# Kernel tuning notes

Measured on AMD Instinct MI355X. Metric: run time of the kernel, lower is better.

## Reference

```python
import jax, jax.numpy as jnp
import numpy as np

INPUT_SIZE = 64
HIDDEN_SIZE = 128
OUTPUT_SIZE = 64


def setup_inputs() -> dict:
    key = jax.random.key(0)
    ks = jax.random.split(key, 7)
    B, T = 256, 2048
    x = jax.random.normal(ks[0], (B, T, INPUT_SIZE), dtype=jnp.float32)
    s_in = 1.0 / np.sqrt(INPUT_SIZE)
    s_h = 1.0 / np.sqrt(HIDDEN_SIZE)
    Wx_w = jax.random.uniform(ks[1], (HIDDEN_SIZE, INPUT_SIZE), minval=-s_in, maxval=s_in, dtype=jnp.float32)
    Wx_b = jax.random.uniform(ks[2], (HIDDEN_SIZE,), minval=-s_in, maxval=s_in, dtype=jnp.float32)
    Wh_w = jax.random.uniform(ks[3], (HIDDEN_SIZE, HIDDEN_SIZE), minval=-s_h, maxval=s_h, dtype=jnp.float32)
    Wh_b = jax.random.uniform(ks[4], (HIDDEN_SIZE,), minval=-s_h, maxval=s_h, dtype=jnp.float32)
    fc_w = jax.random.uniform(ks[5], (OUTPUT_SIZE, HIDDEN_SIZE), minval=-s_h, maxval=s_h, dtype=jnp.float32)
    fc_b = jax.random.uniform(ks[6], (OUTPUT_SIZE,), minval=-s_h, maxval=s_h, dtype=jnp.float32)
    return {"x": x, "Wx_w": Wx_w, "Wx_b": Wx_b, "Wh_w": Wh_w, "Wh_b": Wh_b, "fc_w": fc_w, "fc_b": fc_b}


def reference(x, Wx_w, Wx_b, Wh_w, Wh_b, fc_w, fc_b):
    B = x.shape[0]
    # Precompute the input projection for all timesteps in one big GEMM;
    # the recurrence itself is a scan over time (sequential dependency).
    xt_proj = jnp.einsum('bti,hi->bth', x, Wx_w) + Wx_b  # [B, T, H]

    def step(h, xp):
        h = jnp.tanh(xp + h @ Wh_w.T + Wh_b)
        return h, None

    h0 = jnp.zeros((B, HIDDEN_SIZE), dtype=x.dtype)
    h_final, _ = jax.lax.scan(step, h0, jnp.swapaxes(xt_proj, 0, 1))  # scan over T
    out = h_final @ fc_w.T + fc_b  # [B, O]
    return jax.nn.softmax(out, axis=1)
```

## Files before the change

### kernel.cpp

```cpp
#include <hip/hip_runtime.h>

#define BATCH 256
#define TSTEPS 2048
#define INSZ 64
#define HID 128
#define OUTSZ 64
#define NTHR 512
#define CHUNK 32
#define NCHUNK (TSTEPS / CHUNK)

typedef float v2f __attribute__((ext_vector_type(2)));
typedef float v4f __attribute__((ext_vector_type(4)));

#define AS1 __attribute__((address_space(1)))
#define AS3 __attribute__((address_space(3)))

template <int CTRL>
__device__ __forceinline__ float dppf(float v) {
  return __int_as_float(__builtin_amdgcn_update_dpp(
      0, __float_as_int(v), CTRL, 0xF, 0xF, true));
}
#define DPP_XOR1 0xB1
#define DPP_XOR2 0x4E
#define DPP_XOR15 0x140
#define DPP_XOR8 0x128

__device__ __forceinline__ v2f pk_mul(v2f a, v2f b) {
  v2f d; asm("v_pk_mul_f32 %0, %1, %2" : "=v"(d) : "v"(a), "v"(b)); return d;
}
__device__ __forceinline__ v2f pk_fma(v2f a, v2f b, v2f c) {
  v2f d; asm("v_pk_fma_f32 %0, %1, %2, %3" : "=v"(d) : "v"(a), "v"(b), "v"(c)); return d;
}

__launch_bounds__(NTHR, 1)
__global__ void rnn_dpp512_kernel(const float* __restrict__ x,
                                  const float* __restrict__ Wx_w,
                                  const float* __restrict__ Wx_b,
                                  const float* __restrict__ Wh_w,
                                  const float* __restrict__ Wh_b,
                                  const float* __restrict__ fc_w,
                                  const float* __restrict__ fc_b,
                                  float* __restrict__ out) {
  const int b = blockIdx.x;
  const int tid = threadIdx.x;
  const int s = tid & 15;
  const int g = tid >> 4;
  const int s0 = s & 1, s1 = (s >> 1) & 1, s2 = (s >> 2) & 1;
  const int c = (s0 ^ s2) | ((s1 ^ s2) << 1);
  const int jf = 4 * g + c;
  const int jp = jf + ((jf >> 3) << 2);

  __shared__ __align__(16) float hA[192], hB[192];
  __shared__ __align__(16) float xsm[2][CHUNK * INSZ];

  v2f wh2[4][4], wx2[4][2];
#pragma unroll
  for (int m = 0; m < 4; ++m) {
    const int row = 4 * g + (m ^ c);
    const float* p = Wh_w + row * HID + 8 * s;
    v4f t0 = *(const v4f*)p;
    v4f t1 = *(const v4f*)(p + 4);
    wh2[m][0] = (v2f){t0.x, t0.y};
    wh2[m][1] = (v2f){t0.z, t0.w};
    wh2[m][2] = (v2f){t1.x, t1.y};
    wh2[m][3] = (v2f){t1.z, t1.w};
    const float* q = Wx_w + row * INSZ + 4 * s;
    v4f t2 = *(const v4f*)q;
    wx2[m][0] = (v2f){t2.x, t2.y};
    wx2[m][1] = (v2f){t2.z, t2.w};
  }
  const float bc = Wx_b[jf] + Wh_b[jf];

  const float* xg = x + (size_t)b * TSTEPS * INSZ;

  if (tid < 192) hA[tid] = 0.f;

  {
    const AS1 float* gp = (const AS1 float*)(xg + tid * 4);
    AS3 float* d = (AS3 float*)(&xsm[0][(tid >> 6) * 256]);
    __builtin_amdgcn_global_load_lds(gp, d, 16, 0, 0);
  }
  asm volatile("s_waitcnt vmcnt(0) lgkmcnt(0)\ns_barrier" ::: "memory");

  for (int tc = 0; tc < NCHUNK; ++tc) {
#pragma unroll
    for (int m = 0; m < 4; ++m) {
#pragma unroll
      for (int kk = 0; kk < 4; ++kk) asm("" : "+v"(wh2[m][kk]));
#pragma unroll
      for (int kk = 0; kk < 2; ++kk) asm("" : "+v"(wx2[m][kk]));
    }
    if (tc + 1 < NCHUNK) {
      const AS1 float* gp =
          (const AS1 float*)(xg + (size_t)(tc + 1) * CHUNK * INSZ + tid * 4);
      AS3 float* d = (AS3 float*)(&xsm[(tc + 1) & 1][(tid >> 6) * 256]);
      __builtin_amdgcn_global_load_lds(gp, d, 16, 0, 0);
    }
    const float* xc = xsm[tc & 1];
    v4f xcur = *(const v4f*)&xc[4 * s];

#pragma unroll
    for (int ts = 0; ts < CHUNK; ++ts) {
      const float* hin = (ts & 1) ? hB : hA;
      float* hout = (ts & 1) ? hA : hB;

      const float* hp = hin + 12 * s;
      v4f h0 = *(const v4f*)hp;
      v4f h1 = *(const v4f*)(hp + 4);

      v4f xnext;
      if (ts + 1 < CHUNK) xnext = *(const v4f*)&xc[(ts + 1) * INSZ + 4 * s];

      v2f xx0 = (v2f){xcur.x, xcur.y}, xx1 = (v2f){xcur.z, xcur.w};
      v2f hx0 = (v2f){h0.x, h0.y}, hx1 = (v2f){h0.z, h0.w};
      v2f hx2 = (v2f){h1.x, h1.y}, hx3 = (v2f){h1.z, h1.w};

      float a0, a1, a2, a3;
      float* aptr[4] = {&a0, &a1, &a2, &a3};
#pragma unroll
      for (int m = 0; m < 4; ++m) {
        v2f acc = pk_mul(wx2[m][0], xx0);
        acc = pk_fma(wx2[m][1], xx1, acc);
        acc = pk_fma(wh2[m][0], hx0, acc);
        acc = pk_fma(wh2[m][1], hx1, acc);
        acc = pk_fma(wh2[m][2], hx2, acc);
        acc = pk_fma(wh2[m][3], hx3, acc);
        *aptr[m] = acc.x + acc.y;
      }

      float b0 = a0 + dppf<DPP_XOR1>(a1);
      float b1 = a2 + dppf<DPP_XOR1>(a3);
      float w  = b0 + dppf<DPP_XOR2>(b1);
      float u  = w + dppf<DPP_XOR15>(w);
      float z  = u + dppf<DPP_XOR8>(u);

      z += bc;
      float e = __builtin_amdgcn_exp2f(z * 2.8853900817779268f);
      float hn = fmaf(-2.f, __builtin_amdgcn_rcpf(e + 1.f), 1.f);

      if (s < 4) hout[jp] = hn;

      if (ts + 1 < CHUNK) xcur = xnext;

      if (ts == CHUNK - 1) {
        asm volatile("s_waitcnt vmcnt(0) lgkmcnt(0)\ns_barrier" ::: "memory");
      } else {
        asm volatile("s_waitcnt lgkmcnt(0)\ns_barrier" ::: "memory");
      }
    }
  }

  if (tid < 64) {
    float acc = fc_b[tid];
    const float* fr = fc_w + tid * HID;
#pragma unroll
    for (int k8 = 0; k8 < 16; ++k8) {
      v4f w0 = *(const v4f*)(fr + 8 * k8);
      v4f w1 = *(const v4f*)(fr + 8 * k8 + 4);
      const float* hh = &hA[12 * k8];
      v4f p0 = *(const v4f*)hh;
      v4f p1 = *(const v4f*)(hh + 4);
      acc = fmaf(w0.x, p0.x, acc);
      acc = fmaf(w0.y, p0.y, acc);
      acc = fmaf(w0.z, p0.z, acc);
      acc = fmaf(w0.w, p0.w, acc);
      acc = fmaf(w1.x, p1.x, acc);
      acc = fmaf(w1.y, p1.y, acc);
      acc = fmaf(w1.z, p1.z, acc);
      acc = fmaf(w1.w, p1.w, acc);
    }
    float m = acc;
#pragma unroll
    for (int off = 32; off >= 1; off >>= 1) m = fmaxf(m, __shfl_xor(m, off, 64));
    float e = __builtin_amdgcn_exp2f((acc - m) * 1.4426950408889634f);
    float ssum = e;
#pragma unroll
    for (int off = 32; off >= 1; off >>= 1) ssum += __shfl_xor(ssum, off, 64);
    out[b * OUTSZ + tid] = e / ssum;
  }
}

extern "C" void kernel_launch(void* const* d_in, const int* in_sizes, int n_in,
                              void* d_out, int out_size, void* d_ws, size_t ws_size,
                              hipStream_t stream) {
  const float* x    = (const float*)d_in[0];
  const float* Wx_w = (const float*)d_in[1];
  const float* Wx_b = (const float*)d_in[2];
  const float* Wh_w = (const float*)d_in[3];
  const float* Wh_b = (const float*)d_in[4];
  const float* fc_w = (const float*)d_in[5];
  const float* fc_b = (const float*)d_in[6];
  float* out = (float*)d_out;

  rnn_dpp512_kernel<<<BATCH, NTHR, 0, stream>>>(x, Wx_w, Wx_b, Wh_w, Wh_b, fc_w, fc_b, out);
}
```

Baseline: 538.8 us.

## Stream x directly from global into registers with 4-deep prefetch ring

Replaces the chunked global-to-LDS double buffer for x with per-thread global loads straight into registers, keeping four timesteps in flight and waiting with vmcnt(3) at each step barrier. The goal is to drop the LDS read of x every step and the full vmcnt(0) drain at chunk boundaries. In exchange, every timestep now issues one global load per thread, and the recurrence depends on global latency being hidden by a prefetch distance of only four steps.

New measurement: 613.1 us. 13.8% more time.

```diff
diff --git a/kernel.cpp b/kernel.cpp
--- a/kernel.cpp
+++ b/kernel.cpp
@@ -6,14 +6,9 @@
 #define HID 128
 #define OUTSZ 64
 #define NTHR 512
-#define CHUNK 32
-#define NCHUNK (TSTEPS / CHUNK)
 
 typedef float v2f __attribute__((ext_vector_type(2)));
 typedef float v4f __attribute__((ext_vector_type(4)));
-
-#define AS1 __attribute__((address_space(1)))
-#define AS3 __attribute__((address_space(3)))
 
 template <int CTRL>
 __device__ __forceinline__ float dppf(float v) {
@@ -33,14 +28,14 @@
 }
 
 __launch_bounds__(NTHR, 1)
-__global__ void rnn_dpp512_kernel(const float* __restrict__ x,
-                                  const float* __restrict__ Wx_w,
-                                  const float* __restrict__ Wx_b,
-                                  const float* __restrict__ Wh_w,
-                                  const float* __restrict__ Wh_b,
-                                  const float* __restrict__ fc_w,
-                                  const float* __restrict__ fc_b,
-                                  float* __restrict__ out) {
+__global__ void rnn_gx_kernel(const float* __restrict__ x,
+                              const float* __restrict__ Wx_w,
+                              const float* __restrict__ Wx_b,
+                              const float* __restrict__ Wh_w,
+                              const float* __restrict__ Wh_b,
+                              const float* __restrict__ fc_w,
+                              const float* __restrict__ fc_b,
+                              float* __restrict__ out) {
   const int b = blockIdx.x;
   const int tid = threadIdx.x;
   const int s = tid & 15;
@@ -51,7 +46,6 @@
   const int jp = jf + ((jf >> 3) << 2);
 
   __shared__ __align__(16) float hA[192], hB[192];
-  __shared__ __align__(16) float xsm[2][CHUNK * INSZ];
 
   v2f wh2[4][4], wx2[4][2];
 #pragma unroll
@@ -73,82 +67,73 @@
 
   const float* xg = x + (size_t)b * TSTEPS * INSZ;
 
+  unsigned volim = (TSTEPS - 1) * 256u + 16u * s;
+  unsigned voA = 16u * s;
+  unsigned voB = voA + 256u;
+  unsigned voC = voA + 512u;
+  unsigned voD = voA + 768u;
+  v4f xa, xb, xc_, xd;
+  asm volatile("global_load_dwordx4 %0, %1, %2" : "=v"(xa) : "v"(voA), "s"(xg));
+  asm volatile("global_load_dwordx4 %0, %1, %2" : "=v"(xb) : "v"(voB), "s"(xg));
+  asm volatile("global_load_dwordx4 %0, %1, %2" : "=v"(xc_) : "v"(voC), "s"(xg));
+  asm volatile("global_load_dwordx4 %0, %1, %2" : "=v"(xd) : "v"(voD), "s"(xg));
+
   if (tid < 192) hA[tid] = 0.f;
 
-  {
-    const AS1 float* gp = (const AS1 float*)(xg + tid * 4);
-    AS3 float* d = (AS3 float*)(&xsm[0][(tid >> 6) * 256]);
-    __builtin_amdgcn_global_load_lds(gp, d, 16, 0, 0);
-  }
-  asm volatile("s_waitcnt vmcnt(0) lgkmcnt(0)\ns_barrier" ::: "memory");
+  auto step = [&](const float* hin, float* hout, v4f& xbuf, unsigned& vo) {
+    asm volatile("s_waitcnt vmcnt(3) lgkmcnt(0)\n\ts_barrier"
+                 : "+v"(xbuf) :: "memory");
 
-  for (int tc = 0; tc < NCHUNK; ++tc) {
+    v2f xx0 = (v2f){xbuf.x, xbuf.y}, xx1 = (v2f){xbuf.z, xbuf.w};
+    vo += 1024u;
+    vo = vo < volim ? vo : volim;
+    asm volatile("global_load_dwordx4 %0, %1, %2" : "=v"(xbuf) : "v"(vo), "s"(xg));
+
+    const float* hp = hin + 12 * s;
+    v4f h0 = *(const v4f*)hp;
+    v4f h1 = *(const v4f*)(hp + 4);
+    v2f hx0 = (v2f){h0.x, h0.y}, hx1 = (v2f){h0.z, h0.w};
+    v2f hx2 = (v2f){h1.x, h1.y}, hx3 = (v2f){h1.z, h1.w};
+
+    float a0, a1, a2, a3;
+    float* aptr[4] = {&a0, &a1, &a2, &a3};
 #pragma unroll
     for (int m = 0; m < 4; ++m) {
+      v2f acc = pk_mul(wx2[m][0], xx0);
+      acc = pk_fma(wx2[m][1], xx1, acc);
+      acc = pk_fma(wh2[m][0], hx0, acc);
+      acc = pk_fma(wh2[m][1], hx1, acc);
+      acc = pk_fma(wh2[m][2], hx2, acc);
+      acc = pk_fma(wh2[m][3], hx3, acc);
+      *aptr[m] = acc.x + acc.y;
+    }
+
+    float b0 = a0 + dppf<DPP_XOR1>(a1);
+    float b1 = a2 + dppf<DPP_XOR1>(a3);
+    float w  = b0 + dppf<DPP_XOR2>(b1);
+    float u  = w + dppf<DPP_XOR15>(w);
+    float z  = u + dppf<DPP_XOR8>(u);
+
+    z += bc;
+    float e = __builtin_amdgcn_exp2f(z * 2.8853900817779268f);
+    float hn = fmaf(-2.f, __builtin_amdgcn_rcpf(e + 1.f), 1.f);
+
+    if (s < 4) hout[jp] = hn;
+  };
+
+  for (int t4 = 0; t4 < TSTEPS / 4; ++t4) {
 #pragma unroll
-      for (int kk = 0; kk < 4; ++kk) asm("" : "+v"(wh2[m][kk]));
-#pragma unroll
-      for (int kk = 0; kk < 2; ++kk) asm("" : "+v"(wx2[m][kk]));
+    for (int m = 0; m < 4; ++m) {
+      asm("" : "+v"(wh2[m][0]), "+v"(wh2[m][1]), "+v"(wh2[m][2]), "+v"(wh2[m][3]));
+      asm("" : "+v"(wx2[m][0]), "+v"(wx2[m][1]));
     }
-    if (tc + 1 < NCHUNK) {
-      const AS1 float* gp =
-          (const AS1 float*)(xg + (size_t)(tc + 1) * CHUNK * INSZ + tid * 4);
-      AS3 float* d = (AS3 float*)(&xsm[(tc + 1) & 1][(tid >> 6) * 256]);
-      __builtin_amdgcn_global_load_lds(gp, d, 16, 0, 0);
-    }
-    const float* xc = xsm[tc & 1];
-    v4f xcur = *(const v4f*)&xc[4 * s];
+    step(hA, hB, xa, voA);
+    step(hB, hA, xb, voB);
+    step(hA, hB, xc_, voC);
+    step(hB, hA, xd, voD);
+  }
 
-#pragma unroll
-    for (int ts = 0; ts < CHUNK; ++ts) {
-      const float* hin = (ts & 1) ? hB : hA;
-      float* hout = (ts & 1) ? hA : hB;
-
-      const float* hp = hin + 12 * s;
-      v4f h0 = *(const v4f*)hp;
-      v4f h1 = *(const v4f*)(hp + 4);
-
-      v4f xnext;
-      if (ts + 1 < CHUNK) xnext = *(const v4f*)&xc[(ts + 1) * INSZ + 4 * s];
-
-      v2f xx0 = (v2f){xcur.x, xcur.y}, xx1 = (v2f){xcur.z, xcur.w};
-      v2f hx0 = (v2f){h0.x, h0.y}, hx1 = (v2f){h0.z, h0.w};
-      v2f hx2 = (v2f){h1.x, h1.y}, hx3 = (v2f){h1.z, h1.w};
-
-      float a0, a1, a2, a3;
-      float* aptr[4] = {&a0, &a1, &a2, &a3};
-#pragma unroll
-      for (int m = 0; m < 4; ++m) {
-        v2f acc = pk_mul(wx2[m][0], xx0);
-        acc = pk_fma(wx2[m][1], xx1, acc);
-        acc = pk_fma(wh2[m][0], hx0, acc);
-        acc = pk_fma(wh2[m][1], hx1, acc);
-        acc = pk_fma(wh2[m][2], hx2, acc);
-        acc = pk_fma(wh2[m][3], hx3, acc);
-        *aptr[m] = acc.x + acc.y;
-      }
-
-      float b0 = a0 + dppf<DPP_XOR1>(a1);
-      float b1 = a2 + dppf<DPP_XOR1>(a3);
-      float w  = b0 + dppf<DPP_XOR2>(b1);
-      float u  = w + dppf<DPP_XOR15>(w);
-      float z  = u + dppf<DPP_XOR8>(u);
-
-      z += bc;
-      float e = __builtin_amdgcn_exp2f(z * 2.8853900817779268f);
-      float hn = fmaf(-2.f, __builtin_amdgcn_rcpf(e + 1.f), 1.f);
-
-      if (s < 4) hout[jp] = hn;
-
-      if (ts + 1 < CHUNK) xcur = xnext;
-
-      if (ts == CHUNK - 1) {
-        asm volatile("s_waitcnt vmcnt(0) lgkmcnt(0)\ns_barrier" ::: "memory");
-      } else {
-        asm volatile("s_waitcnt lgkmcnt(0)\ns_barrier" ::: "memory");
-      }
-    }
-  }
+  asm volatile("s_waitcnt vmcnt(0) lgkmcnt(0)\n\ts_barrier" ::: "memory");
 
   if (tid < 64) {
     float acc = fc_b[tid];
@@ -192,5 +177,5 @@
   const float* fc_b = (const float*)d_in[6];
   float* out = (float*)d_out;
 
-  rnn_dpp512_kernel<<<BATCH, NTHR, 0, stream>>>(x, Wx_w, Wx_b, Wh_w, Wh_b, fc_w, fc_b, out);
+  rnn_gx_kernel<<<BATCH, NTHR, 0, stream>>>(x, Wx_w, Wx_b, Wh_w, Wh_b, fc_w, fc_b, out);
 }
```

## Split K across 32 lanes with 8 rows per group and swizzle reduction

Applied to the files above, without the earlier changes.

Reassigns work so each group of 32 lanes handles 8 hidden rows, with each lane covering a K-slice of 4 hidden and 2 input elements instead of 8 and 4. Per-step LDS reads shrink to one v4f of h and one v2f of x per lane, and FMA chains shorten. In exchange the reduction gains an extra level done with ds_swizzle across 16 lanes, which goes through the LDS crossbar and adds latency on the serial critical path. The empty asm register-pinning statements are also removed.

Measured after the change: 643.6 us. +19.4%, slower.

```diff
diff --git a/kernel.cpp b/kernel.cpp
--- a/kernel.cpp
+++ b/kernel.cpp
@@ -25,6 +25,10 @@
 #define DPP_XOR15 0x140
 #define DPP_XOR8 0x128
 
+__device__ __forceinline__ float swz16(float v) {
+  return __int_as_float(__builtin_amdgcn_ds_swizzle(__float_as_int(v), 0x401F));
+}
+
 __device__ __forceinline__ v2f pk_mul(v2f a, v2f b) {
   v2f d; asm("v_pk_mul_f32 %0, %1, %2" : "=v"(d) : "v"(a), "v"(b)); return d;
 }
@@ -33,41 +37,40 @@
 }
 
 __launch_bounds__(NTHR, 1)
-__global__ void rnn_dpp512_kernel(const float* __restrict__ x,
-                                  const float* __restrict__ Wx_w,
-                                  const float* __restrict__ Wx_b,
-                                  const float* __restrict__ Wh_w,
-                                  const float* __restrict__ Wh_b,
-                                  const float* __restrict__ fc_w,
-                                  const float* __restrict__ fc_b,
-                                  float* __restrict__ out) {
+__global__ void rnn_kt4b_kernel(const float* __restrict__ x,
+                                const float* __restrict__ Wx_w,
+                                const float* __restrict__ Wx_b,
+                                const float* __restrict__ Wh_w,
+                                const float* __restrict__ Wh_b,
+                                const float* __restrict__ fc_w,
+                                const float* __restrict__ fc_b,
+                                float* __restrict__ out) {
   const int b = blockIdx.x;
   const int tid = threadIdx.x;
-  const int s = tid & 15;
-  const int g = tid >> 4;
-  const int s0 = s & 1, s1 = (s >> 1) & 1, s2 = (s >> 2) & 1;
-  const int c = (s0 ^ s2) | ((s1 ^ s2) << 1);
-  const int jf = 4 * g + c;
-  const int jp = jf + ((jf >> 3) << 2);
+  const int lane = tid & 63;
+  const int wave = tid >> 6;
+  const int n0 = lane & 1, n1 = (lane >> 1) & 1, n2 = (lane >> 2) & 1;
+  const int b4 = (lane >> 4) & 1;
+  const int s = lane & 31;
+  const int g = (wave << 1) | ((lane >> 5) & 1);
+  const int f = (n0 ^ n2) | ((n1 ^ n2) << 1) | (b4 << 2);
+  const int jf = 8 * g + f;
+  const int jp = 12 * g + f;
+  const int hoff = 4 * s + ((s >> 1) << 2);
 
   __shared__ __align__(16) float hA[192], hB[192];
   __shared__ __align__(16) float xsm[2][CHUNK * INSZ];
 
-  v2f wh2[4][4], wx2[4][2];
+  v2f wh2[8][2], wx2[8];
 #pragma unroll
-  for (int m = 0; m < 4; ++m) {
-    const int row = 4 * g + (m ^ c);
-    const float* p = Wh_w + row * HID + 8 * s;
+  for (int m = 0; m < 8; ++m) {
+    const int row = 8 * g + (m ^ f);
+    const float* p = Wh_w + row * HID + 4 * s;
     v4f t0 = *(const v4f*)p;
-    v4f t1 = *(const v4f*)(p + 4);
     wh2[m][0] = (v2f){t0.x, t0.y};
     wh2[m][1] = (v2f){t0.z, t0.w};
-    wh2[m][2] = (v2f){t1.x, t1.y};
-    wh2[m][3] = (v2f){t1.z, t1.w};
-    const float* q = Wx_w + row * INSZ + 4 * s;
-    v4f t2 = *(const v4f*)q;
-    wx2[m][0] = (v2f){t2.x, t2.y};
-    wx2[m][1] = (v2f){t2.z, t2.w};
+    const float* q = Wx_w + row * INSZ + 2 * s;
+    wx2[m] = *(const v2f*)q;
   }
   const float bc = Wx_b[jf] + Wh_b[jf];
 
@@ -83,13 +86,6 @@
   asm volatile("s_waitcnt vmcnt(0) lgkmcnt(0)\ns_barrier" ::: "memory");
 
   for (int tc = 0; tc < NCHUNK; ++tc) {
-#pragma unroll
-    for (int m = 0; m < 4; ++m) {
-#pragma unroll
-      for (int kk = 0; kk < 4; ++kk) asm("" : "+v"(wh2[m][kk]));
-#pragma unroll
-      for (int kk = 0; kk < 2; ++kk) asm("" : "+v"(wx2[m][kk]));
-    }
     if (tc + 1 < NCHUNK) {
       const AS1 float* gp =
           (const AS1 float*)(xg + (size_t)(tc + 1) * CHUNK * INSZ + tid * 4);
@@ -97,48 +93,45 @@
       __builtin_amdgcn_global_load_lds(gp, d, 16, 0, 0);
     }
     const float* xc = xsm[tc & 1];
-    v4f xcur = *(const v4f*)&xc[4 * s];
+    v2f xcur = *(const v2f*)&xc[2 * s];
 
 #pragma unroll
     for (int ts = 0; ts < CHUNK; ++ts) {
       const float* hin = (ts & 1) ? hB : hA;
       float* hout = (ts & 1) ? hA : hB;
 
-      const float* hp = hin + 12 * s;
-      v4f h0 = *(const v4f*)hp;
-      v4f h1 = *(const v4f*)(hp + 4);
+      v4f h0 = *(const v4f*)(hin + hoff);
 
-      v4f xnext;
-      if (ts + 1 < CHUNK) xnext = *(const v4f*)&xc[(ts + 1) * INSZ + 4 * s];
+      v2f xnext;
+      if (ts + 1 < CHUNK) xnext = *(const v2f*)&xc[(ts + 1) * INSZ + 2 * s];
 
-      v2f xx0 = (v2f){xcur.x, xcur.y}, xx1 = (v2f){xcur.z, xcur.w};
       v2f hx0 = (v2f){h0.x, h0.y}, hx1 = (v2f){h0.z, h0.w};
-      v2f hx2 = (v2f){h1.x, h1.y}, hx3 = (v2f){h1.z, h1.w};
 
-      float a0, a1, a2, a3;
-      float* aptr[4] = {&a0, &a1, &a2, &a3};
+      float a0, a1, a2, a3, a4, a5, a6, a7;
+      float* aptr[8] = {&a0, &a1, &a2, &a3, &a4, &a5, &a6, &a7};
 #pragma unroll
-      for (int m = 0; m < 4; ++m) {
-        v2f acc = pk_mul(wx2[m][0], xx0);
-        acc = pk_fma(wx2[m][1], xx1, acc);
+      for (int m = 0; m < 8; ++m) {
+        v2f acc = pk_mul(wx2[m], xcur);
         acc = pk_fma(wh2[m][0], hx0, acc);
         acc = pk_fma(wh2[m][1], hx1, acc);
-        acc = pk_fma(wh2[m][2], hx2, acc);
-        acc = pk_fma(wh2[m][3], hx3, acc);
         *aptr[m] = acc.x + acc.y;
       }
 
       float b0 = a0 + dppf<DPP_XOR1>(a1);
       float b1 = a2 + dppf<DPP_XOR1>(a3);
-      float w  = b0 + dppf<DPP_XOR2>(b1);
-      float u  = w + dppf<DPP_XOR15>(w);
-      float z  = u + dppf<DPP_XOR8>(u);
+      float b2 = a4 + dppf<DPP_XOR1>(a5);
+      float b3 = a6 + dppf<DPP_XOR1>(a7);
+      float c0 = b0 + dppf<DPP_XOR2>(b1);
+      float c1 = b2 + dppf<DPP_XOR2>(b3);
+      float d0 = c0 + swz16(c1);
+      float e0 = d0 + dppf<DPP_XOR15>(d0);
+      float z  = e0 + dppf<DPP_XOR8>(e0);
 
       z += bc;
       float e = __builtin_amdgcn_exp2f(z * 2.8853900817779268f);
       float hn = fmaf(-2.f, __builtin_amdgcn_rcpf(e + 1.f), 1.f);
 
-      if (s < 4) hout[jp] = hn;
+      if ((lane & 12) == 0) hout[jp] = hn;
 
       if (ts + 1 < CHUNK) xcur = xnext;
 
@@ -192,5 +185,5 @@
   const float* fc_b = (const float*)d_in[6];
   float* out = (float*)d_out;
 
-  rnn_dpp512_kernel<<<BATCH, NTHR, 0, stream>>>(x, Wx_w, Wx_b, Wh_w, Wh_b, fc_w, fc_b, out);
+  rnn_kt4b_kernel<<<BATCH, NTHR, 0, stream>>>(x, Wx_w, Wx_b, Wh_w, Wh_b, fc_w, fc_b, out);
 }
```
